# Performance work log

Measured on AMD Instinct MI355X. Metric: run time of the kernel, lower is better.

Reference implementation:

```python
import jax, jax.numpy as jnp
import numpy as np

NUM_HEADS = 16
KEY_DEPTH = 1024


def setup_inputs() -> dict:
    key = jax.random.key(0)
    ks = jax.random.split(key, 7)
    B, L, D = 2, 2048, 1024
    scale = 1.0 / np.sqrt(D)
    return {
        "query_antecedent": jax.random.normal(ks[0], (B, L, D), jnp.float32),
        "memory_antecedent": jax.random.normal(ks[1], (B, L, D), jnp.float32),
        "bias": jax.random.normal(ks[2], (1, 1, L, L), jnp.float32),
        "Wq": jax.random.normal(ks[3], (D, KEY_DEPTH), jnp.float32) * scale,
        "Wk": jax.random.normal(ks[4], (D, KEY_DEPTH), jnp.float32) * scale,
        "Wv": jax.random.normal(ks[5], (D, KEY_DEPTH), jnp.float32) * scale,
        "Wo": jax.random.normal(ks[6], (KEY_DEPTH, D), jnp.float32) * scale,
    }


def _split_heads(x, h):
    # [B, L, D] -> [B, H, L, D/H]
    b, l, d = x.shape
    return x.reshape(b, l, h, d // h).transpose(0, 2, 1, 3)


def reference(query_antecedent, memory_antecedent, bias, Wq, Wk, Wv, Wo):
    h = NUM_HEADS
    d_head = KEY_DEPTH // h
    q = _split_heads(query_antecedent @ Wq, h) * (d_head ** -0.5)
    k = _split_heads(memory_antecedent @ Wk, h)
    v = _split_heads(memory_antecedent @ Wv, h)
    # [B, H, Lq, Lk]
    logits = jnp.einsum("bhqd,bhkd->bhqk", q, k) + bias
    weights = jax.nn.softmax(logits, axis=-1)
    x = jnp.einsum("bhqk,bhkd->bhqd", weights, v)
    # combine heads: [B, H, L, d] -> [B, L, H*d]
    b, _, l, d = x.shape
    x = x.transpose(0, 2, 1, 3).reshape(b, l, h * d)
    return x @ Wo
```

## Files before the change

### kernel.cpp

```cpp
#include <hip/hip_runtime.h>
#include <hip/hip_bf16.h>


typedef __attribute__((ext_vector_type(8))) short short8;
typedef __attribute__((ext_vector_type(4))) float float4v;

#define BATCH 2
#define LSEQ 2048
#define DMODEL 1024
#define NHEADS 16
#define DHEAD 64
#define MROWS 4096
#define QKVLD 3072

__global__ __launch_bounds__(256)
void convert_kernel(const float* __restrict__ qa, const float* __restrict__ ma,
                    __hip_bfloat16* __restrict__ qo, __hip_bfloat16* __restrict__ mo)
{
    const size_t i = ((size_t)blockIdx.x * 256 + threadIdx.x) * 8;
    const float* src = blockIdx.y ? ma : qa;
    __hip_bfloat16* dst = blockIdx.y ? mo : qo;
    float4 v0 = *reinterpret_cast<const float4*>(src + i);
    float4 v1 = *reinterpret_cast<const float4*>(src + i + 4);
    union { __hip_bfloat16 h[8]; int4 v; } pk;
    pk.h[0] = (__hip_bfloat16)v0.x; pk.h[1] = (__hip_bfloat16)v0.y;
    pk.h[2] = (__hip_bfloat16)v0.z; pk.h[3] = (__hip_bfloat16)v0.w;
    pk.h[4] = (__hip_bfloat16)v1.x; pk.h[5] = (__hip_bfloat16)v1.y;
    pk.h[6] = (__hip_bfloat16)v1.z; pk.h[7] = (__hip_bfloat16)v1.w;
    *reinterpret_cast<int4*>(dst + i) = pk.v;
}

__global__ __launch_bounds__(256)
void transpose_w_kernel(const float* __restrict__ W0, const float* __restrict__ W1,
                        const float* __restrict__ W2, const float* __restrict__ W3,
                        __hip_bfloat16* __restrict__ T0, __hip_bfloat16* __restrict__ T1,
                        __hip_bfloat16* __restrict__ T2, __hip_bfloat16* __restrict__ T3)
{
    __shared__ __hip_bfloat16 T[64][68];

    const float* W; __hip_bfloat16* D;
    if      (blockIdx.z == 0) { W = W0; D = T0; }
    else if (blockIdx.z == 1) { W = W1; D = T1; }
    else if (blockIdx.z == 2) { W = W2; D = T2; }
    else                      { W = W3; D = T3; }

    const int t  = threadIdx.x;
    const int n0 = blockIdx.x * 64;
    const int k0 = blockIdx.y * 64;

#pragma unroll
    for (int p = 0; p < 4; ++p) {
        const int r = p * 16 + (t >> 4);
        const int c = (t & 15) * 4;
        float4 v = *reinterpret_cast<const float4*>(&W[(size_t)(k0 + r) * DMODEL + n0 + c]);
        union { __hip_bfloat16 h[4]; ushort4 v; } pk;
        pk.h[0] = (__hip_bfloat16)v.x; pk.h[1] = (__hip_bfloat16)v.y;
        pk.h[2] = (__hip_bfloat16)v.z; pk.h[3] = (__hip_bfloat16)v.w;
        *reinterpret_cast<ushort4*>(&T[r][c]) = pk.v;
    }
    __syncthreads();
#pragma unroll
    for (int p = 0; p < 2; ++p) {
        const int n  = p * 32 + (t & 31);
        const int kc = (t >> 5) * 8;
        union { __hip_bfloat16 h[8]; int4 v; } pk;
#pragma unroll
        for (int j = 0; j < 8; ++j) pk.h[j] = T[kc + j][n];
        *reinterpret_cast<int4*>(&D[(size_t)(n0 + n) * DMODEL + k0 + kc]) = pk.v;
    }
}

__global__ __launch_bounds__(256)
void gemm_bt_kernel(const __hip_bfloat16* __restrict__ A0,
                    const __hip_bfloat16* __restrict__ A1, int nsplit,
                    float alpha0, float alpha1,
                    const __hip_bfloat16* __restrict__ Bt,
                    float* __restrict__ Cf, __hip_bfloat16* __restrict__ Cb,
                    int K, int ldc)
{
    __shared__ __hip_bfloat16 As[128][40];
    __shared__ __hip_bfloat16 Bs[128][40];

    const int t    = threadIdx.x;
    const int w    = t >> 6;
    const int lane = t & 63;
    const int l15  = lane & 15;
    const int lq   = lane >> 4;
    const int m0   = blockIdx.y * 128;
    const int n0   = blockIdx.x * 128;
    const int wm   = (w >> 1) * 64;
    const int wn   = (w & 1) * 64;
    const int sr   = t >> 1;
    const int sc   = (t & 1) * 16;

    const __hip_bfloat16* A = (n0 < nsplit) ? A0 : A1;
    const float alpha = (n0 < nsplit) ? alpha0 : alpha1;

    float4v acc[4][4];
#pragma unroll
    for (int mi = 0; mi < 4; ++mi)
#pragma unroll
        for (int ni = 0; ni < 4; ++ni) acc[mi][ni] = (float4v){0.f, 0.f, 0.f, 0.f};

    const __hip_bfloat16* Arow = A  + (size_t)(m0 + sr) * K + sc;
    const __hip_bfloat16* Brow = Bt + (size_t)(n0 + sr) * K + sc;

    int4 a0 = *reinterpret_cast<const int4*>(Arow);
    int4 a1 = *reinterpret_cast<const int4*>(Arow + 8);
    int4 b0 = *reinterpret_cast<const int4*>(Brow);
    int4 b1 = *reinterpret_cast<const int4*>(Brow + 8);

    for (int k0 = 0; k0 < K; k0 += 32) {
        __syncthreads();
        *reinterpret_cast<int4*>(&As[sr][sc])     = a0;
        *reinterpret_cast<int4*>(&As[sr][sc + 8]) = a1;
        *reinterpret_cast<int4*>(&Bs[sr][sc])     = b0;
        *reinterpret_cast<int4*>(&Bs[sr][sc + 8]) = b1;
        const int kn = (k0 + 32 < K) ? k0 + 32 : k0;
        a0 = *reinterpret_cast<const int4*>(Arow + kn);
        a1 = *reinterpret_cast<const int4*>(Arow + kn + 8);
        b0 = *reinterpret_cast<const int4*>(Brow + kn);
        b1 = *reinterpret_cast<const int4*>(Brow + kn + 8);
        __syncthreads();

        short8 af[4], bf[4];
#pragma unroll
        for (int mi = 0; mi < 4; ++mi)
            af[mi] = *reinterpret_cast<const short8*>(&As[wm + mi * 16 + l15][lq * 8]);
#pragma unroll
        for (int ni = 0; ni < 4; ++ni)
            bf[ni] = *reinterpret_cast<const short8*>(&Bs[wn + ni * 16 + l15][lq * 8]);
#pragma unroll
        for (int mi = 0; mi < 4; ++mi)
#pragma unroll
            for (int ni = 0; ni < 4; ++ni)
                acc[mi][ni] = __builtin_amdgcn_mfma_f32_16x16x32_bf16(
                    af[mi], bf[ni], acc[mi][ni], 0, 0, 0);
    }

#pragma unroll
    for (int mi = 0; mi < 4; ++mi)
#pragma unroll
        for (int ni = 0; ni < 4; ++ni)
#pragma unroll
            for (int r = 0; r < 4; ++r) {
                const int row = m0 + wm + mi * 16 + lq * 4 + r;
                const int col = n0 + wn + ni * 16 + l15;
                const float v = acc[mi][ni][r] * alpha;
                if (Cf) Cf[(size_t)row * ldc + col] = v;
                else    Cb[(size_t)row * ldc + col] = (__hip_bfloat16)v;
            }
}

#define KSTR 68
#define PSTR 132

__global__ __launch_bounds__(256)
void attn_mfma_kernel(const __hip_bfloat16* __restrict__ QKV,
                      const float* __restrict__ bias,
                      __hip_bfloat16* __restrict__ X)
{
    __shared__ __hip_bfloat16 Ks[128][KSTR];
    __shared__ __hip_bfloat16 Vt[64][PSTR];
    __shared__ __hip_bfloat16 Ps[4][32][PSTR];

    const int t   = threadIdx.x;
    const int w   = t >> 6;
    const int l15 = t & 15;
    const int lq  = (t & 63) >> 4;

    const int bid = blockIdx.x;
    const int r8  = bid & 7;
    const int j   = bid >> 3;
    const int bh  = r8 + 8 * (j >> 4);
    const int q0  = (j & 15) * 128;
    const int b   = bh >> 4;
    const int h   = bh & 15;

    const __hip_bfloat16* Kb = QKV + (size_t)b * LSEQ * QKVLD + 1024 + h * DHEAD;
    const __hip_bfloat16* Vb = Kb + 1024;

    short8 aq[2][2];
#pragma unroll
    for (int g = 0; g < 2; ++g) {
        const __hip_bfloat16* qrow = QKV +
            (size_t)(b * LSEQ + q0 + w * 32 + g * 16 + l15) * QKVLD + h * DHEAD + lq * 8;
        aq[g][0] = *reinterpret_cast<const short8*>(qrow);
        aq[g][1] = *reinterpret_cast<const short8*>(qrow + 32);
    }

    float lpart[2][4];
    float4v o_acc[2][4];
#pragma unroll
    for (int g = 0; g < 2; ++g)
#pragma unroll
        for (int r = 0; r < 4; ++r) lpart[g][r] = 0.f;
#pragma unroll
    for (int g = 0; g < 2; ++g)
#pragma unroll
        for (int n = 0; n < 4; ++n) o_acc[g][n] = (float4v){0.f, 0.f, 0.f, 0.f};

    const int skey = t >> 2;
    const int sdh  = (t & 3) * 16;
    const int g2   = t & 3;

    int4 pk[2][2], pv[2][2];
#pragma unroll
    for (int rnd = 0; rnd < 2; ++rnd) {
        const int key = rnd * 64 + skey;
        const __hip_bfloat16* ks = Kb + (size_t)key * QKVLD + sdh;
        pk[rnd][0] = *reinterpret_cast<const int4*>(ks);
        pk[rnd][1] = *reinterpret_cast<const int4*>(ks + 8);
        const __hip_bfloat16* vs = Vb + (size_t)key * QKVLD + sdh;
        pv[rnd][0] = *reinterpret_cast<const int4*>(vs);
        pv[rnd][1] = *reinterpret_cast<const int4*>(vs + 8);
    }

    for (int kt = 0; kt < LSEQ / 128; ++kt) {
        const int k0 = kt * 128;
        __syncthreads();
#pragma unroll
        for (int rnd = 0; rnd < 2; ++rnd) {
            const int key = rnd * 64 + skey;
            *reinterpret_cast<int4*>(&Ks[key][sdh])     = pk[rnd][0];
            *reinterpret_cast<int4*>(&Ks[key][sdh + 8]) = pk[rnd][1];
            const __hip_bfloat16* vp0 = reinterpret_cast<const __hip_bfloat16*>(&pv[rnd][0]);
            const __hip_bfloat16* vp1 = reinterpret_cast<const __hip_bfloat16*>(&pv[rnd][1]);
            const int vcol = (((key >> 3) ^ g2) << 3) + (key & 7);
#pragma unroll
            for (int jj = 0; jj < 8; ++jj) Vt[sdh + jj][vcol]     = vp0[jj];
#pragma unroll
            for (int jj = 0; jj < 8; ++jj) Vt[sdh + 8 + jj][vcol] = vp1[jj];
        }
        {
            const int knext = (kt + 1 < LSEQ / 128) ? k0 + 128 : k0;
#pragma unroll
            for (int rnd = 0; rnd < 2; ++rnd) {
                const int key = knext + rnd * 64 + skey;
                const __hip_bfloat16* ks = Kb + (size_t)key * QKVLD + sdh;
                pk[rnd][0] = *reinterpret_cast<const int4*>(ks);
                pk[rnd][1] = *reinterpret_cast<const int4*>(ks + 8);
                const __hip_bfloat16* vs = Vb + (size_t)key * QKVLD + sdh;
                pv[rnd][0] = *reinterpret_cast<const int4*>(vs);
                pv[rnd][1] = *reinterpret_cast<const int4*>(vs + 8);
            }
        }
        __syncthreads();

        float4v s0[8], s1[8];
#pragma unroll
        for (int c = 0; c < 8; ++c) {
            s0[c] = (float4v){0.f, 0.f, 0.f, 0.f};
            s1[c] = (float4v){0.f, 0.f, 0.f, 0.f};
        }
#pragma unroll
        for (int c = 0; c < 8; ++c) {
            short8 bk0 = *reinterpret_cast<const short8*>(&Ks[c * 16 + l15][lq * 8]);
            short8 bk1 = *reinterpret_cast<const short8*>(&Ks[c * 16 + l15][32 + lq * 8]);
            s0[c] = __builtin_amdgcn_mfma_f32_16x16x32_bf16(aq[0][0], bk0, s0[c], 0, 0, 0);
            s0[c] = __builtin_amdgcn_mfma_f32_16x16x32_bf16(aq[0][1], bk1, s0[c], 0, 0, 0);
            s1[c] = __builtin_amdgcn_mfma_f32_16x16x32_bf16(aq[1][0], bk0, s1[c], 0, 0, 0);
            s1[c] = __builtin_amdgcn_mfma_f32_16x16x32_bf16(aq[1][1], bk1, s1[c], 0, 0, 0);
        }

#pragma unroll
        for (int g = 0; g < 2; ++g) {
            float4v* s = g ? s1 : s0;
            const float* bp = bias +
                (size_t)(q0 + w * 32 + g * 16 + lq * 4) * LSEQ + l15;
            float bv[8][4];
#pragma unroll
            for (int c = 0; c < 8; ++c)
#pragma unroll
                for (int r = 0; r < 4; ++r)
                    bv[c][r] = bp[(size_t)r * LSEQ + k0 + c * 16];
#pragma unroll
            for (int c = 0; c < 8; ++c)
#pragma unroll
                for (int r = 0; r < 4; ++r) {
                    const float p = __expf(s[c][r] + bv[c][r]);
                    lpart[g][r] += p;
                    Ps[w][g * 16 + lq * 4 + r][c * 16 + l15] = (__hip_bfloat16)p;
                }
        }

        asm volatile("s_waitcnt lgkmcnt(0)" ::: "memory");

#pragma unroll
        for (int kc = 0; kc < 4; ++kc) {
            short8 vt[4];
#pragma unroll
            for (int n = 0; n < 4; ++n) {
                const int blk = (kc * 4 + lq) ^ n;
                vt[n] = *reinterpret_cast<const short8*>(&Vt[n * 16 + l15][blk << 3]);
            }
#pragma unroll
            for (int g = 0; g < 2; ++g) {
                short8 ap = *reinterpret_cast<const short8*>(
                    &Ps[w][g * 16 + l15][kc * 32 + lq * 8]);
#pragma unroll
                for (int n = 0; n < 4; ++n)
                    o_acc[g][n] = __builtin_amdgcn_mfma_f32_16x16x32_bf16(
                        ap, vt[n], o_acc[g][n], 0, 0, 0);
            }
        }
    }

#pragma unroll
    for (int g = 0; g < 2; ++g)
#pragma unroll
        for (int r = 0; r < 4; ++r) {
#pragma unroll
            for (int off = 1; off < 16; off <<= 1)
                lpart[g][r] += __shfl_xor(lpart[g][r], off);
        }

#pragma unroll
    for (int g = 0; g < 2; ++g) {
        float inv[4];
#pragma unroll
        for (int r = 0; r < 4; ++r) inv[r] = 1.f / lpart[g][r];
#pragma unroll
        for (int n = 0; n < 4; ++n)
#pragma unroll
            for (int r = 0; r < 4; ++r)
                Ps[w][g * 16 + lq * 4 + r][n * 16 + l15] =
                    (__hip_bfloat16)(o_acc[g][n][r] * inv[r]);
    }
    asm volatile("s_waitcnt lgkmcnt(0)" ::: "memory");
    {
        const int lane = t & 63;
        const int rr   = lane >> 2;
        const int cc   = (lane & 3) * 16;
#pragma unroll
        for (int g = 0; g < 2; ++g) {
            const int row = q0 + w * 32 + g * 16 + rr;
            __hip_bfloat16* dst =
                X + (size_t)(b * LSEQ + row) * DMODEL + h * DHEAD + cc;
            *reinterpret_cast<int4*>(dst) =
                *reinterpret_cast<const int4*>(&Ps[w][g * 16 + rr][cc]);
            *reinterpret_cast<int4*>(dst + 8) =
                *reinterpret_cast<const int4*>(&Ps[w][g * 16 + rr][cc + 8]);
        }
    }
}

extern "C" void kernel_launch(void* const* d_in, const int* in_sizes, int n_in,
                              void* d_out, int out_size, void* d_ws, size_t ws_size,
                              hipStream_t stream)
{
    const float* qa   = (const float*)d_in[0];
    const float* ma   = (const float*)d_in[1];
    const float* bias = (const float*)d_in[2];
    const float* Wq   = (const float*)d_in[3];
    const float* Wk   = (const float*)d_in[4];
    const float* Wv   = (const float*)d_in[5];
    const float* Wo   = (const float*)d_in[6];
    float* out = (float*)d_out;

    char* wsb = (char*)d_ws;
    __hip_bfloat16* qa16 = (__hip_bfloat16*)(wsb);
    __hip_bfloat16* ma16 = (__hip_bfloat16*)(wsb + (8u << 20));
    __hip_bfloat16* Wt   = (__hip_bfloat16*)(wsb + (16u << 20));
    __hip_bfloat16* Wot  = (__hip_bfloat16*)(wsb + (22u << 20));
    __hip_bfloat16* QKVw = (__hip_bfloat16*)(wsb + (24u << 20));
    __hip_bfloat16* Xw   = qa16;

    convert_kernel<<<dim3(MROWS * DMODEL / (256 * 8), 2), 256, 0, stream>>>(
        qa, ma, qa16, ma16);

    transpose_w_kernel<<<dim3(16, 16, 4), 256, 0, stream>>>(
        Wq, Wk, Wv, Wo,
        Wt, Wt + (size_t)DMODEL * DMODEL, Wt + 2 * (size_t)DMODEL * DMODEL, Wot);

    gemm_bt_kernel<<<dim3(QKVLD / 128, MROWS / 128), 256, 0, stream>>>(
        qa16, ma16, DMODEL, 0.125f, 1.0f, Wt, nullptr, QKVw, DMODEL, QKVLD);

    attn_mfma_kernel<<<dim3(512), 256, 0, stream>>>(QKVw, bias, Xw);

    gemm_bt_kernel<<<dim3(DMODEL / 128, MROWS / 128), 256, 0, stream>>>(
        Xw, Xw, DMODEL + 1, 1.0f, 1.0f, Wot, out, nullptr, DMODEL, DMODEL);
}
```

Baseline: 278.2 us.

## Keep softmax probabilities in registers via transposed MFMA, drop P shared buffer

Computes S^T by swapping MFMA operands so each lane holds a row's probabilities in the layout needed as the B operand of the PV MFMA. This removes the Ps shared-memory round trip and its waitcnt, and turns the bias reads into vectorized float4 loads. The V tile reads are adjusted to match the new key ordering, and the output is written straight from registers. It also adds s_setprio around the MFMA blocks and shrinks LDS use, at the cost of more intricate index math.

```diff
diff --git a/kernel.cpp b/kernel.cpp
--- a/kernel.cpp
+++ b/kernel.cpp
@@ -3,6 +3,7 @@
 
 
 typedef __attribute__((ext_vector_type(8))) short short8;
+typedef __attribute__((ext_vector_type(4))) short short4v;
 typedef __attribute__((ext_vector_type(4))) float float4v;
 
 #define BATCH 2
@@ -162,7 +163,6 @@
 {
     __shared__ __hip_bfloat16 Ks[128][KSTR];
     __shared__ __hip_bfloat16 Vt[64][PSTR];
-    __shared__ __hip_bfloat16 Ps[4][32][PSTR];
 
     const int t   = threadIdx.x;
     const int w   = t >> 6;
@@ -189,12 +189,11 @@
         aq[g][1] = *reinterpret_cast<const short8*>(qrow + 32);
     }
 
-    float lpart[2][4];
+    const float* bp0 = bias + (size_t)(q0 + w * 32 + l15) * LSEQ + lq * 4;
+    const float* bp1 = bp0 + (size_t)16 * LSEQ;
+
+    float lsum[2] = {0.f, 0.f};
     float4v o_acc[2][4];
-#pragma unroll
-    for (int g = 0; g < 2; ++g)
-#pragma unroll
-        for (int r = 0; r < 4; ++r) lpart[g][r] = 0.f;
 #pragma unroll
     for (int g = 0; g < 2; ++g)
 #pragma unroll
@@ -247,100 +246,84 @@
         }
         __syncthreads();
 
-        float4v s0[8], s1[8];
-#pragma unroll
-        for (int c = 0; c < 8; ++c) {
-            s0[c] = (float4v){0.f, 0.f, 0.f, 0.f};
-            s1[c] = (float4v){0.f, 0.f, 0.f, 0.f};
-        }
-#pragma unroll
-        for (int c = 0; c < 8; ++c) {
-            short8 bk0 = *reinterpret_cast<const short8*>(&Ks[c * 16 + l15][lq * 8]);
-            short8 bk1 = *reinterpret_cast<const short8*>(&Ks[c * 16 + l15][32 + lq * 8]);
-            s0[c] = __builtin_amdgcn_mfma_f32_16x16x32_bf16(aq[0][0], bk0, s0[c], 0, 0, 0);
-            s0[c] = __builtin_amdgcn_mfma_f32_16x16x32_bf16(aq[0][1], bk1, s0[c], 0, 0, 0);
-            s1[c] = __builtin_amdgcn_mfma_f32_16x16x32_bf16(aq[1][0], bk0, s1[c], 0, 0, 0);
-            s1[c] = __builtin_amdgcn_mfma_f32_16x16x32_bf16(aq[1][1], bk1, s1[c], 0, 0, 0);
-        }
-
-#pragma unroll
-        for (int g = 0; g < 2; ++g) {
-            float4v* s = g ? s1 : s0;
-            const float* bp = bias +
-                (size_t)(q0 + w * 32 + g * 16 + lq * 4) * LSEQ + l15;
-            float bv[8][4];
-#pragma unroll
-            for (int c = 0; c < 8; ++c)
-#pragma unroll
-                for (int r = 0; r < 4; ++r)
-                    bv[c][r] = bp[(size_t)r * LSEQ + k0 + c * 16];
-#pragma unroll
-            for (int c = 0; c < 8; ++c)
+#pragma unroll
+        for (int m = 0; m < 4; ++m) {
+            short8 bkA0 = *reinterpret_cast<const short8*>(&Ks[(2*m)    *16 + l15][lq * 8]);
+            short8 bkA1 = *reinterpret_cast<const short8*>(&Ks[(2*m)    *16 + l15][32 + lq * 8]);
+            short8 bkB0 = *reinterpret_cast<const short8*>(&Ks[(2*m + 1)*16 + l15][lq * 8]);
+            short8 bkB1 = *reinterpret_cast<const short8*>(&Ks[(2*m + 1)*16 + l15][32 + lq * 8]);
+            float4v sA[2], sB[2];
+#pragma unroll
+            for (int g = 0; g < 2; ++g) {
+                sA[g] = (float4v){0.f, 0.f, 0.f, 0.f};
+                sB[g] = (float4v){0.f, 0.f, 0.f, 0.f};
+            }
+            __builtin_amdgcn_s_setprio(1);
+#pragma unroll
+            for (int g = 0; g < 2; ++g) {
+                sA[g] = __builtin_amdgcn_mfma_f32_16x16x32_bf16(bkA0, aq[g][0], sA[g], 0, 0, 0);
+                sA[g] = __builtin_amdgcn_mfma_f32_16x16x32_bf16(bkA1, aq[g][1], sA[g], 0, 0, 0);
+                sB[g] = __builtin_amdgcn_mfma_f32_16x16x32_bf16(bkB0, aq[g][0], sB[g], 0, 0, 0);
+                sB[g] = __builtin_amdgcn_mfma_f32_16x16x32_bf16(bkB1, aq[g][1], sB[g], 0, 0, 0);
+            }
+            __builtin_amdgcn_s_setprio(0);
+
+            short8 pf[2];
+#pragma unroll
+            for (int g = 0; g < 2; ++g) {
+                const float* bp = g ? bp1 : bp0;
+                float4v bvA = *reinterpret_cast<const float4v*>(bp + k0 + (2*m)     * 16);
+                float4v bvB = *reinterpret_cast<const float4v*>(bp + k0 + (2*m + 1) * 16);
+                union { __hip_bfloat16 hh[8]; short8 v; } pp;
 #pragma unroll
                 for (int r = 0; r < 4; ++r) {
-                    const float p = __expf(s[c][r] + bv[c][r]);
-                    lpart[g][r] += p;
-                    Ps[w][g * 16 + lq * 4 + r][c * 16 + l15] = (__hip_bfloat16)p;
+                    const float e = __expf(sA[g][r] + bvA[r]);
+                    lsum[g] += e;
+                    pp.hh[r] = (__hip_bfloat16)e;
                 }
-        }
-
-        asm volatile("s_waitcnt lgkmcnt(0)" ::: "memory");
-
-#pragma unroll
-        for (int kc = 0; kc < 4; ++kc) {
+#pragma unroll
+                for (int r = 0; r < 4; ++r) {
+                    const float e = __expf(sB[g][r] + bvB[r]);
+                    lsum[g] += e;
+                    pp.hh[4 + r] = (__hip_bfloat16)e;
+                }
+                pf[g] = pp.v;
+            }
+
             short8 vt[4];
 #pragma unroll
             for (int n = 0; n < 4; ++n) {
-                const int blk = (kc * 4 + lq) ^ n;
-                vt[n] = *reinterpret_cast<const short8*>(&Vt[n * 16 + l15][blk << 3]);
-            }
-#pragma unroll
-            for (int g = 0; g < 2; ++g) {
-                short8 ap = *reinterpret_cast<const short8*>(
-                    &Ps[w][g * 16 + l15][kc * 32 + lq * 8]);
+                const int c0 = (((4*m +     (lq >> 1)) ^ n) << 3) + ((lq & 1) << 2);
+                const int c1 = (((4*m + 2 + (lq >> 1)) ^ n) << 3) + ((lq & 1) << 2);
+                union { short4v h[2]; short8 v; } u;
+                u.h[0] = *reinterpret_cast<const short4v*>(&Vt[n * 16 + l15][c0]);
+                u.h[1] = *reinterpret_cast<const short4v*>(&Vt[n * 16 + l15][c1]);
+                vt[n] = u.v;
+            }
+            __builtin_amdgcn_s_setprio(1);
+#pragma unroll
+            for (int g = 0; g < 2; ++g)
 #pragma unroll
                 for (int n = 0; n < 4; ++n)
                     o_acc[g][n] = __builtin_amdgcn_mfma_f32_16x16x32_bf16(
-                        ap, vt[n], o_acc[g][n], 0, 0, 0);
-            }
+                        vt[n], pf[g], o_acc[g][n], 0, 0, 0);
+            __builtin_amdgcn_s_setprio(0);
         }
     }
 
 #pragma unroll
-    for (int g = 0; g < 2; ++g)
-#pragma unroll
-        for (int r = 0; r < 4; ++r) {
-#pragma unroll
-            for (int off = 1; off < 16; off <<= 1)
-                lpart[g][r] += __shfl_xor(lpart[g][r], off);
-        }
-
-#pragma unroll
     for (int g = 0; g < 2; ++g) {
-        float inv[4];
-#pragma unroll
-        for (int r = 0; r < 4; ++r) inv[r] = 1.f / lpart[g][r];
-#pragma unroll
-        for (int n = 0; n < 4; ++n)
-#pragma unroll
-            for (int r = 0; r < 4; ++r)
-                Ps[w][g * 16 + lq * 4 + r][n * 16 + l15] =
-                    (__hip_bfloat16)(o_acc[g][n][r] * inv[r]);
-    }
-    asm volatile("s_waitcnt lgkmcnt(0)" ::: "memory");
-    {
-        const int lane = t & 63;
-        const int rr   = lane >> 2;
-        const int cc   = (lane & 3) * 16;
-#pragma unroll
-        for (int g = 0; g < 2; ++g) {
-            const int row = q0 + w * 32 + g * 16 + rr;
-            __hip_bfloat16* dst =
-                X + (size_t)(b * LSEQ + row) * DMODEL + h * DHEAD + cc;
-            *reinterpret_cast<int4*>(dst) =
-                *reinterpret_cast<const int4*>(&Ps[w][g * 16 + rr][cc]);
-            *reinterpret_cast<int4*>(dst + 8) =
-                *reinterpret_cast<const int4*>(&Ps[w][g * 16 + rr][cc + 8]);
+        lsum[g] += __shfl_xor(lsum[g], 16);
+        lsum[g] += __shfl_xor(lsum[g], 32);
+        const float inv = 1.f / lsum[g];
+        const int row = q0 + w * 32 + g * 16 + l15;
+        __hip_bfloat16* dst = X + (size_t)(b * LSEQ + row) * DMODEL + h * DHEAD + lq * 4;
+#pragma unroll
+        for (int n = 0; n < 4; ++n) {
+            union { __hip_bfloat16 hh[4]; short4v v; } o;
+#pragma unroll
+            for (int r = 0; r < 4; ++r) o.hh[r] = (__hip_bfloat16)(o_acc[g][n][r] * inv);
+            *reinterpret_cast<short4v*>(dst + n * 16) = o.v;
         }
     }
 }
```

Result: slower. 287.5 us (+3.3%).
